# Performance work log

Hardware: AMD Instinct MI355X
Metric: run time of the kernel (lower is better)

## Reference

```python
import jax, jax.numpy as jnp
import numpy as np

WS = 8                      # window_size
N = WS * WS                 # 64, Householder dimension
PAD = WS - 1                # reflect-pad total (7)
PAD_LO, PAD_HI = PAD // 2, PAD - PAD // 2  # (3, 4)


def setup_inputs() -> dict:
    key = jax.random.key(0)
    k1, k2 = jax.random.split(key)
    x = jax.random.normal(k1, (2, 8, 256, 256), dtype=jnp.float32)
    v = jax.random.normal(k2, (N, N), dtype=jnp.float32)  # 64 Householder vectors (rows)
    return {"x": x, "v": v}


def _get_A(v):
    # A = prod_i (I - 2 v_i v_i^T / ||v_i||^2), composed left-to-right as in the torch loop.
    # A @ (I - 2 v v^T / s) == A - (2/s) * (A v) v^T  -> rank-1 update per step.
    n = v.shape[-1]
    def step(A, vi):
        s = jnp.sum(vi * vi)
        Av = A @ vi                      # [n]
        return A - (2.0 / s) * jnp.outer(Av, vi), None
    A, _ = jax.lax.scan(step, jnp.eye(n, dtype=v.dtype), v)
    return A


def reference(x, v):
    b, c, H, W = x.shape
    xi = x.reshape(b * c, 1, H, W)
    # reflect padding (3,4) on both spatial dims, as in F.pad(..., mode='reflect')
    xp = jnp.pad(xi, ((0, 0), (0, 0), (PAD_LO, PAD_HI), (PAD_LO, PAD_HI)), mode='reflect')
    # unfold: kernel=8, stride=1, padding=0 -> [bc, 64, H, W] (C=1 so channel ordering matches torch)
    patches = jax.lax.conv_general_dilated_patches(
        xp, filter_shape=(WS, WS), window_strides=(1, 1), padding='VALID')
    cols = patches.reshape(b * c, N, H * W)          # [bc, 64, L]
    A = _get_A(v)                                     # [64, 64]
    # OrthoT1d(dim=1): transpose(1,-1) @ A, transpose back -> out[b,m,l] = sum_k cols[b,k,l] A[k,m]
    out = jnp.einsum('bkl,km->bml', cols, A)          # [bc, 64, L]
    # rearrange 'b (h w) (k1 k2) -> b (h w) k1 k2' with k1=H, k2=W
    return out.reshape(b * c, N, H, W)
```

## Files before the change

### kernel.cpp

```cpp
#include <hip/hip_runtime.h>

#define HSZ 256
#define WSZ 256
#define BC  16
#define NCH 64
#define PADLO 3

#define TW 64
#define TH 8
#define NTHR 256
#define TR 15
#define TC 71
#define TSTRIDE 80

typedef short bf16x8 __attribute__((ext_vector_type(8)));
typedef float f32x4  __attribute__((ext_vector_type(4)));

__device__ __forceinline__ int reflect_idx(int i) {
    i = (i < 0) ? -i : i;
    i = (i >= HSZ) ? (2 * (HSZ - 1) - i) : i;
    return i;
}

__device__ __forceinline__ unsigned short f2bf(float f) {
    unsigned u = __builtin_bit_cast(unsigned, f);
    u += 0x7FFFu + ((u >> 16) & 1u);
    return (unsigned short)(u >> 16);
}

__global__ void build_A_frags(const float* __restrict__ v,
                              unsigned short* __restrict__ frags) {
    __shared__ float vs[64][64];
    __shared__ float rs[64];
    __shared__ float As[64][64];

    const int t = threadIdx.x;
    const int w = t >> 6;
    const int l = t & 63;
    const int r = (w << 4) | (l & 15);
    const int q = l >> 4;

    for (int idx = t; idx < 64 * 64; idx += NTHR)
        ((float*)vs)[idx] = v[idx];
    __syncthreads();

    if (t < 64) {
        const f32x4* vp = (const f32x4*)vs[t];
        float s0 = 0, s1 = 0, s2 = 0, s3 = 0;
#pragma unroll
        for (int c = 0; c < 4; ++c) {
            f32x4 vq = vp[c * 4 + 0];
            (void)vq;
        }
        float ss[4] = {0, 0, 0, 0};
#pragma unroll
        for (int c = 0; c < 16; ++c) {
            f32x4 vq = vp[c];
            ss[c & 3] = fmaf(vq[0], vq[0], ss[c & 3]);
            ss[c & 3] = fmaf(vq[1], vq[1], ss[c & 3]);
            ss[c & 3] = fmaf(vq[2], vq[2], ss[c & 3]);
            ss[c & 3] = fmaf(vq[3], vq[3], ss[c & 3]);
        }
        rs[t] = 2.0f / ((ss[0] + ss[1]) + (ss[2] + ss[3]));
    }

    float row[16];
#pragma unroll
    for (int c = 0; c < 16; ++c) row[c] = (q * 16 + c == r) ? 1.0f : 0.0f;

    __syncthreads();

    const f32x4* vq0 = (const f32x4*)&vs[0][q * 16];
    f32x4 nv0 = vq0[0], nv1 = vq0[1], nv2 = vq0[2], nv3 = vq0[3];
    float nrs = rs[0];

    for (int i = 0; i < 64; ++i) {
        f32x4 c0 = nv0, c1 = nv1, c2 = nv2, c3 = nv3;
        const float rcur = nrs;
        if (i < 63) {
            const f32x4* vqn = (const f32x4*)&vs[i + 1][q * 16];
            nv0 = vqn[0]; nv1 = vqn[1]; nv2 = vqn[2]; nv3 = vqn[3];
            nrs = rs[i + 1];
        }
        float vv[16];
#pragma unroll
        for (int j = 0; j < 4; ++j) { vv[j] = c0[j]; vv[4+j] = c1[j]; vv[8+j] = c2[j]; vv[12+j] = c3[j]; }

        float a0 = 0, a1 = 0, a2 = 0, a3 = 0;
#pragma unroll
        for (int c = 0; c < 4; ++c) {
            a0 = fmaf(row[c],      vv[c],      a0);
            a1 = fmaf(row[4 + c],  vv[4 + c],  a1);
            a2 = fmaf(row[8 + c],  vv[8 + c],  a2);
            a3 = fmaf(row[12 + c], vv[12 + c], a3);
        }
        float av = (a0 + a1) + (a2 + a3);
        av += __shfl_xor(av, 16);
        av += __shfl_xor(av, 32);

        const float scale = av * rcur;
#pragma unroll
        for (int c = 0; c < 16; ++c) row[c] = fmaf(-scale, vv[c], row[c]);
    }
#pragma unroll
    for (int c = 0; c < 16; ++c) As[r][q * 16 + c] = row[c];
    __syncthreads();

    const int ln = l & 15, lh = l >> 4;
    const int mb = w;
#pragma unroll
    for (int c2 = 0; c2 < 2; ++c2)
#pragma unroll
        for (int j = 0; j < 8; ++j) {
            float val = As[c2 * 32 + lh * 8 + j][mb * 16 + ln];
            frags[(((mb * 2 + c2) * 64) + l) * 8 + j] = f2bf(val);
        }
}

__global__ __launch_bounds__(256)
void ortho_mfma_kernel(const float* __restrict__ x,
                       const unsigned short* __restrict__ frags,
                       float* __restrict__ out) {
    __shared__ float tile[TR][TSTRIDE];

    const int b  = blockIdx.z;
    const int y0 = blockIdx.y * TH;
    const int x0 = blockIdx.x * TW;
    const float* __restrict__ xb = x + (size_t)b * (HSZ * WSZ);

    const int tx = threadIdx.x;
    const int ty = threadIdx.y;
    const int tid = ty * TW + tx;

    for (int idx = tid; idx < TR * TC; idx += NTHR) {
        const int r  = idx / TC;
        const int c  = idx - r * TC;
        tile[r][c] = xb[reflect_idx(y0 + r - PADLO) * WSZ + reflect_idx(x0 + c - PADLO)];
    }

    const int ln = tx & 15, lh = tx >> 4;

    bf16x8 af[4][2];
#pragma unroll
    for (int mb = 0; mb < 4; ++mb)
#pragma unroll
        for (int c = 0; c < 2; ++c)
            af[mb][c] = *(const bf16x8*)(frags + ((mb * 2 + c) * 64 + tx) * 8);

    __syncthreads();

#pragma unroll
    for (int ry = 0; ry < 2; ++ry) {
        const int tyr = ty * 2 + ry;
        const int y   = y0 + tyr;

        unsigned short bfv[2][16];
#pragma unroll
        for (int c = 0; c < 2; ++c) {
            const f32x4* rp = (const f32x4*)&tile[tyr + 4 * c + lh][4 * ln];
            f32x4 q0 = rp[0], q1 = rp[1], q2 = rp[2], q3 = rp[3];
            float fl[16];
#pragma unroll
            for (int j = 0; j < 4; ++j) { fl[j] = q0[j]; fl[4+j] = q1[j]; fl[8+j] = q2[j]; fl[12+j] = q3[j]; }
#pragma unroll
            for (int j = 0; j < 16; ++j) bfv[c][j] = f2bf(fl[j]);
        }

        bf16x8 bfrag[2][4];
#pragma unroll
        for (int c = 0; c < 2; ++c)
#pragma unroll
            for (int g = 0; g < 4; ++g)
#pragma unroll
                for (int j = 0; j < 8; ++j)
                    bfrag[c][g][j] = (short)bfv[c][g + j];

        float* __restrict__ outb =
            out + (size_t)b * NCH * (HSZ * WSZ) + (size_t)y * WSZ + x0 + 4 * ln;

#pragma unroll
        for (int mb = 0; mb < 4; ++mb) {
            f32x4 acc[4];
#pragma unroll
            for (int g = 0; g < 4; ++g) {
                acc[g] = (f32x4){0.0f, 0.0f, 0.0f, 0.0f};
                acc[g] = __builtin_amdgcn_mfma_f32_16x16x32_bf16(af[mb][0], bfrag[0][g], acc[g], 0, 0, 0);
                acc[g] = __builtin_amdgcn_mfma_f32_16x16x32_bf16(af[mb][1], bfrag[1][g], acc[g], 0, 0, 0);
            }
#pragma unroll
            for (int r = 0; r < 4; ++r) {
                const int ch = mb * 16 + lh * 4 + r;
                f32x4 vv = { acc[0][r], acc[1][r], acc[2][r], acc[3][r] };
                __builtin_nontemporal_store(vv, (f32x4*)&outb[(size_t)ch * (HSZ * WSZ)]);
            }
        }
    }
}

extern "C" void kernel_launch(void* const* d_in, const int* in_sizes, int n_in,
                              void* d_out, int out_size, void* d_ws, size_t ws_size,
                              hipStream_t stream) {
    const float* x = (const float*)d_in[0];
    const float* v = (const float*)d_in[1];
    float* outp = (float*)d_out;
    unsigned short* frags = (unsigned short*)d_ws;

    build_A_frags<<<1, 256, 0, stream>>>(v, frags);

    dim3 grid(WSZ / TW, HSZ / TH, BC);
    dim3 block(TW, TH / 2);
    ortho_mfma_kernel<<<grid, block, 0, stream>>>(x, frags, outp);
}
```

Before: 71.16 us.

## Split work per 16-channel group with full-width row strips and XCD-aware block mapping

After: 68.41 us. 3.9% less time.

```diff
diff --git a/kernel.cpp b/kernel.cpp
--- a/kernel.cpp
+++ b/kernel.cpp
@@ -4,14 +4,14 @@
 #define WSZ 256
 #define BC  16
 #define NCH 64
+#define HW  (HSZ * WSZ)
 #define PADLO 3
 
-#define TW 64
-#define TH 8
+#define SR 16
 #define NTHR 256
-#define TR 15
-#define TC 71
-#define TSTRIDE 80
+#define TR (SR + 7)
+#define TC (WSZ + 7)
+#define TSTRIDE 272
 
 typedef short bf16x8 __attribute__((ext_vector_type(8)));
 typedef float f32x4  __attribute__((ext_vector_type(4)));
@@ -46,12 +46,6 @@
 
     if (t < 64) {
         const f32x4* vp = (const f32x4*)vs[t];
-        float s0 = 0, s1 = 0, s2 = 0, s3 = 0;
-#pragma unroll
-        for (int c = 0; c < 4; ++c) {
-            f32x4 vq = vp[c * 4 + 0];
-            (void)vq;
-        }
         float ss[4] = {0, 0, 0, 0};
 #pragma unroll
         for (int c = 0; c < 16; ++c) {
@@ -118,80 +112,81 @@
 }
 
 __global__ __launch_bounds__(256)
-void ortho_mfma_kernel(const float* __restrict__ x,
-                       const unsigned short* __restrict__ frags,
-                       float* __restrict__ out) {
+void ortho_mfma_plane(const float* __restrict__ x,
+                      const unsigned short* __restrict__ frags,
+                      float* __restrict__ out) {
     __shared__ float tile[TR][TSTRIDE];
 
-    const int b  = blockIdx.z;
-    const int y0 = blockIdx.y * TH;
-    const int x0 = blockIdx.x * TW;
-    const float* __restrict__ xb = x + (size_t)b * (HSZ * WSZ);
+    const int bid = blockIdx.x;
+    const int lid = (bid & 7) * 128 + (bid >> 3);
+    const int b   = lid >> 6;
+    const int rem = lid & 63;
+    const int mb  = rem >> 4;
+    const int ys  = rem & 15;
+    const int y0  = ys * SR;
+
+    const float* __restrict__ xb = x + (size_t)b * HW;
 
     const int tx = threadIdx.x;
-    const int ty = threadIdx.y;
-    const int tid = ty * TW + tx;
+    const int wv = threadIdx.y;
+    const int tid = wv * 64 + tx;
 
     for (int idx = tid; idx < TR * TC; idx += NTHR) {
-        const int r  = idx / TC;
-        const int c  = idx - r * TC;
-        tile[r][c] = xb[reflect_idx(y0 + r - PADLO) * WSZ + reflect_idx(x0 + c - PADLO)];
+        const int r = idx / TC;
+        const int c = idx - r * TC;
+        tile[r][c] = xb[(size_t)reflect_idx(y0 + r - PADLO) * WSZ + reflect_idx(c - PADLO)];
     }
 
     const int ln = tx & 15, lh = tx >> 4;
 
-    bf16x8 af[4][2];
-#pragma unroll
-    for (int mb = 0; mb < 4; ++mb)
-#pragma unroll
-        for (int c = 0; c < 2; ++c)
-            af[mb][c] = *(const bf16x8*)(frags + ((mb * 2 + c) * 64 + tx) * 8);
-
-    __syncthreads();
-
-#pragma unroll
-    for (int ry = 0; ry < 2; ++ry) {
-        const int tyr = ty * 2 + ry;
+    const bf16x8 af0 = *(const bf16x8*)(frags + ((mb * 2 + 0) * 64 + tx) * 8);
+    const bf16x8 af1 = *(const bf16x8*)(frags + ((mb * 2 + 1) * 64 + tx) * 8);
+
+    __syncthreads();
+
+    float* __restrict__ outp = out + (size_t)(b * NCH + mb * 16) * HW;
+
+#pragma unroll
+    for (int rr = 0; rr < 4; ++rr) {
+        const int tyr = wv * 4 + rr;
         const int y   = y0 + tyr;
 
-        unsigned short bfv[2][16];
-#pragma unroll
-        for (int c = 0; c < 2; ++c) {
-            const f32x4* rp = (const f32x4*)&tile[tyr + 4 * c + lh][4 * ln];
-            f32x4 q0 = rp[0], q1 = rp[1], q2 = rp[2], q3 = rp[3];
-            float fl[16];
-#pragma unroll
-            for (int j = 0; j < 4; ++j) { fl[j] = q0[j]; fl[4+j] = q1[j]; fl[8+j] = q2[j]; fl[12+j] = q3[j]; }
-#pragma unroll
-            for (int j = 0; j < 16; ++j) bfv[c][j] = f2bf(fl[j]);
-        }
-
-        bf16x8 bfrag[2][4];
-#pragma unroll
-        for (int c = 0; c < 2; ++c)
-#pragma unroll
-            for (int g = 0; g < 4; ++g)
-#pragma unroll
-                for (int j = 0; j < 8; ++j)
-                    bfrag[c][g][j] = (short)bfv[c][g + j];
-
-        float* __restrict__ outb =
-            out + (size_t)b * NCH * (HSZ * WSZ) + (size_t)y * WSZ + x0 + 4 * ln;
-
-#pragma unroll
-        for (int mb = 0; mb < 4; ++mb) {
+#pragma unroll
+        for (int qq = 0; qq < 4; ++qq) {
+            unsigned short bfv[2][16];
+#pragma unroll
+            for (int c = 0; c < 2; ++c) {
+                const f32x4* rp = (const f32x4*)&tile[tyr + 4 * c + lh][64 * qq + 4 * ln];
+                f32x4 q0 = rp[0], q1 = rp[1], q2 = rp[2], q3 = rp[3];
+                float fl[16];
+#pragma unroll
+                for (int j = 0; j < 4; ++j) { fl[j] = q0[j]; fl[4+j] = q1[j]; fl[8+j] = q2[j]; fl[12+j] = q3[j]; }
+#pragma unroll
+                for (int j = 0; j < 16; ++j) bfv[c][j] = f2bf(fl[j]);
+            }
+
+            bf16x8 bfrag[2][4];
+#pragma unroll
+            for (int c = 0; c < 2; ++c)
+#pragma unroll
+                for (int g = 0; g < 4; ++g)
+#pragma unroll
+                    for (int j = 0; j < 8; ++j)
+                        bfrag[c][g][j] = (short)bfv[c][g + j];
+
             f32x4 acc[4];
 #pragma unroll
             for (int g = 0; g < 4; ++g) {
                 acc[g] = (f32x4){0.0f, 0.0f, 0.0f, 0.0f};
-                acc[g] = __builtin_amdgcn_mfma_f32_16x16x32_bf16(af[mb][0], bfrag[0][g], acc[g], 0, 0, 0);
-                acc[g] = __builtin_amdgcn_mfma_f32_16x16x32_bf16(af[mb][1], bfrag[1][g], acc[g], 0, 0, 0);
+                acc[g] = __builtin_amdgcn_mfma_f32_16x16x32_bf16(af0, bfrag[0][g], acc[g], 0, 0, 0);
+                acc[g] = __builtin_amdgcn_mfma_f32_16x16x32_bf16(af1, bfrag[1][g], acc[g], 0, 0, 0);
             }
+
 #pragma unroll
             for (int r = 0; r < 4; ++r) {
-                const int ch = mb * 16 + lh * 4 + r;
+                const int chl = lh * 4 + r;
                 f32x4 vv = { acc[0][r], acc[1][r], acc[2][r], acc[3][r] };
-                __builtin_nontemporal_store(vv, (f32x4*)&outb[(size_t)ch * (HSZ * WSZ)]);
+                *(f32x4*)&outp[(size_t)chl * HW + (size_t)y * WSZ + 64 * qq + 4 * ln] = vv;
             }
         }
     }
@@ -207,7 +202,7 @@
 
     build_A_frags<<<1, 256, 0, stream>>>(v, frags);
 
-    dim3 grid(WSZ / TW, HSZ / TH, BC);
-    dim3 block(TW, TH / 2);
-    ortho_mfma_kernel<<<grid, block, 0, stream>>>(x, frags, outp);
-}
+    dim3 grid(BC * 4 * 16);
+    dim3 block(64, 4);
+    ortho_mfma_plane<<<grid, block, 0, stream>>>(x, frags, outp);
+}
```
